# Kernel optimization log

Hardware: AMD Instinct MI355X
Metric: run time of the kernel (lower is better)

Reference implementation:

```python
import jax, jax.numpy as jnp
import numpy as np

GROUPS = 32
EPS = 1e-5


def group_norm(x, gamma, beta):
    # x: [B, C, H, W]; normalize over (C//G, H, W) within each of G groups
    B, C, H, W = x.shape
    xg = x.reshape(B, GROUPS, C // GROUPS, H, W)
    mean = xg.mean(axis=(2, 3, 4), keepdims=True)
    var = xg.var(axis=(2, 3, 4), keepdims=True)
    xg = (xg - mean) * jax.lax.rsqrt(var + EPS)
    x = xg.reshape(B, C, H, W)
    return x * gamma[None, :, None, None] + beta[None, :, None, None]


def conv1x1(x, W, b):
    # 1x1 conv == pointwise linear over channels. x: [B,C,H,W], W: [Cout,Cin]
    return jnp.einsum('oc,bchw->bohw', W, x) + b[None, :, None, None]


def setup_inputs() -> dict:
    key = jax.random.key(0)
    ks = jax.random.split(key, 6)
    B, C, H, W = 16, 512, 32, 32
    scale = 1.0 / np.sqrt(C)  # ~kaiming-ish init for 1x1 convs
    return {
        'x': jax.random.normal(ks[0], (B, C, H, W), jnp.float32),
        'gn_gamma': jnp.ones((C,), jnp.float32),
        'gn_beta': jnp.zeros((C,), jnp.float32),
        'Wq': jax.random.normal(ks[1], (C, C), jnp.float32) * scale,
        'bq': jnp.zeros((C,), jnp.float32),
        'Wk': jax.random.normal(ks[2], (C, C), jnp.float32) * scale,
        'bk': jnp.zeros((C,), jnp.float32),
        'Wv': jax.random.normal(ks[3], (C, C), jnp.float32) * scale,
        'bv': jnp.zeros((C,), jnp.float32),
        'Wp': jax.random.normal(ks[4], (C, C), jnp.float32) * scale,
        'bp': jnp.zeros((C,), jnp.float32),
    }


def reference(x, gn_gamma, gn_beta, Wq, bq, Wk, bk, Wv, bv, Wp, bp):
    B, C, H, W = x.shape
    h = group_norm(x, gn_gamma, gn_beta)
    q = conv1x1(h, Wq, bq).reshape(B, C, H * W)  # [B,C,T]
    k = conv1x1(h, Wk, bk).reshape(B, C, H * W)
    v = conv1x1(h, Wv, bv).reshape(B, C, H * W)
    # scores [B, T(query), S(key)] = q^T k, scaled by C^{-1/2}
    w = jnp.einsum('bct,bcs->bts', q, k) * (C ** -0.5)
    w = jax.nn.softmax(w, axis=-1)
    h = jnp.einsum('bts,bcs->bct', w, v).reshape(B, C, H, W)
    h = conv1x1(h, Wp, bp)
    return x + h
```

## Files before the change

### kernel.cpp

```cpp
#include <hip/hip_runtime.h>

typedef unsigned short u16;
typedef __bf16 bf16x8 __attribute__((ext_vector_type(8)));
typedef float f32x16 __attribute__((ext_vector_type(16)));

__device__ __forceinline__ u16 f2bf(float f) {
    unsigned u = __builtin_bit_cast(unsigned, f);
    u += 0x7fffu + ((u >> 16) & 1u);
    return (u16)(u >> 16);
}
__device__ __forceinline__ float bf2f(u16 h) {
    return __builtin_bit_cast(float, (unsigned)h << 16);
}

#define GLDS16(g, l) __builtin_amdgcn_global_load_lds( \
    (const __attribute__((address_space(1))) void*)(g), \
    (__attribute__((address_space(3))) void*)(l), 16, 0, 0)

#define QK_SCALE 0.044194173824159216f

__global__ __launch_bounds__(256) void convert_kernel(
    const float* __restrict__ Wq, const float* __restrict__ Wk,
    const float* __restrict__ Wv, const float* __restrict__ Wp,
    const float* __restrict__ bq, const float* __restrict__ bk,
    const float* __restrict__ bv,
    u16* __restrict__ Wqkv, u16* __restrict__ Wpb, float* __restrict__ bqkv)
{
    int idx = blockIdx.x * 256 + threadIdx.x;
    if (idx < 786432) {
        int which = idx >> 18;
        int off   = idx & 262143;
        if (which == 0)
            Wqkv[idx] = f2bf(Wq[off] * QK_SCALE);
        else
            Wqkv[idx] = f2bf(((which == 1) ? Wk : Wv)[off]);
    } else {
        int off = idx - 786432;
        Wpb[off] = f2bf(Wp[off]);
    }
    if (idx < 1536) {
        float bvv = (idx < 512) ? bq[idx] * QK_SCALE
                  : (idx < 1024) ? bk[idx & 511] : bv[idx & 511];
        bqkv[idx] = bvv;
    }
}

__global__ __launch_bounds__(256) void gn_kernel(
    const float* __restrict__ x, const float* __restrict__ gamma,
    const float* __restrict__ beta, u16* __restrict__ ht)
{
    const int g = blockIdx.x, b = blockIdx.y, tid = threadIdx.x;
    const float* xg = x + ((size_t)b * 512 + (size_t)g * 16) * 1024;

    float s = 0.f, s2 = 0.f;
    const float4* x4 = (const float4*)xg;
    #pragma unroll 4
    for (int i = tid; i < 4096; i += 256) {
        float4 v = x4[i];
        s  += v.x + v.y + v.z + v.w;
        s2 += v.x * v.x + v.y * v.y + v.z * v.z + v.w * v.w;
    }
    #pragma unroll
    for (int off = 32; off; off >>= 1) {
        s  += __shfl_down(s, off);
        s2 += __shfl_down(s2, off);
    }
    __shared__ float rs[4], rs2[4];
    __shared__ float stat[2];
    const int w = tid >> 6;
    if ((tid & 63) == 0) { rs[w] = s; rs2[w] = s2; }
    __syncthreads();
    if (tid == 0) {
        float S  = rs[0] + rs[1] + rs[2] + rs[3];
        float S2 = rs2[0] + rs2[1] + rs2[2] + rs2[3];
        float mean = S * (1.f / 16384.f);
        float var  = S2 * (1.f / 16384.f) - mean * mean;
        stat[0] = mean;
        stat[1] = rsqrtf(var + 1e-5f);
    }
    __syncthreads();
    const float mean = stat[0], rstd = stat[1];

    float ga[16], be[16];
    #pragma unroll
    for (int ci = 0; ci < 16; ci++) {
        ga[ci] = gamma[g * 16 + ci];
        be[ci] = beta[g * 16 + ci];
    }
    for (int t = tid; t < 1024; t += 256) {
        u16 yv[16];
        #pragma unroll
        for (int ci = 0; ci < 16; ci++) {
            float v = xg[ci * 1024 + t];
            yv[ci] = f2bf((v - mean) * rstd * ga[ci] + be[ci]);
        }
        uint4* dst = (uint4*)(ht + ((size_t)b * 1024 + t) * 512 + g * 16);
        dst[0] = ((const uint4*)yv)[0];
        dst[1] = ((const uint4*)yv)[1];
    }
}

__global__ __launch_bounds__(256) void softmax_kernel(u16* __restrict__ scores)
{
    const int row  = blockIdx.x * 4 + (threadIdx.x >> 6);
    const int lane = threadIdx.x & 63;
    u16* p = scores + (size_t)row * 1024 + lane * 16;

    uint4 w0 = ((const uint4*)p)[0];
    uint4 w1 = ((const uint4*)p)[1];
    unsigned wd[8] = {w0.x, w0.y, w0.z, w0.w, w1.x, w1.y, w1.z, w1.w};
    float v[16];
    #pragma unroll
    for (int i = 0; i < 8; i++) {
        v[2 * i]     = __builtin_bit_cast(float, wd[i] << 16);
        v[2 * i + 1] = __builtin_bit_cast(float, wd[i] & 0xffff0000u);
    }
    float m = v[0];
    #pragma unroll
    for (int i = 1; i < 16; i++) m = fmaxf(m, v[i]);
    #pragma unroll
    for (int off = 1; off < 64; off <<= 1) m = fmaxf(m, __shfl_xor(m, off));

    float s = 0.f;
    #pragma unroll
    for (int i = 0; i < 16; i++) { v[i] = __expf(v[i] - m); s += v[i]; }
    #pragma unroll
    for (int off = 1; off < 64; off <<= 1) s += __shfl_xor(s, off);
    const float inv = 1.0f / s;

    #pragma unroll
    for (int i = 0; i < 8; i++) {
        unsigned lo = f2bf(v[2 * i] * inv);
        unsigned hi = f2bf(v[2 * i + 1] * inv);
        wd[i] = lo | (hi << 16);
    }
    ((uint4*)p)[0] = make_uint4(wd[0], wd[1], wd[2], wd[3]);
    ((uint4*)p)[1] = make_uint4(wd[4], wd[5], wd[6], wd[7]);
}

template <int MODE>
__global__ __launch_bounds__(256) void gemm_nt(
    const u16* __restrict__ A, const u16* __restrict__ B,
    size_t strideA, size_t strideB, int lda, int ldb, int K,
    u16* __restrict__ o0, u16* __restrict__ o1, u16* __restrict__ o2,
    float* __restrict__ fo, const float* __restrict__ bias,
    const float* __restrict__ xres)
{
    __shared__ u16 As[128 * 64];
    __shared__ u16 Bs[128 * 64];

    const int tid   = threadIdx.x;
    const int lane  = tid & 63;
    const int wave  = tid >> 6;
    const int wm    = (wave >> 1) * 64;
    const int wn    = (wave & 1) * 64;
    const int l31   = lane & 31;
    const int khalf = lane >> 5;
    const int b     = blockIdx.z;

    const u16* Ab = A + (size_t)b * strideA + (size_t)blockIdx.y * 128 * lda;
    const u16* Bb = B + (size_t)b * strideB + (size_t)blockIdx.x * 128 * ldb;

    const int srow = lane >> 3;
    const int sc   = lane & 7;
    const int scg  = sc ^ srow;

    f32x16 acc[2][2] = {};

    for (int k0 = 0; k0 < K; k0 += 64) {
        __syncthreads();
        #pragma unroll
        for (int s = 0; s < 4; s++) {
            const int r = wave * 32 + s * 8 + srow;
            GLDS16(Ab + (size_t)r * lda + k0 + scg * 8, As + r * 64 + sc * 8);
            GLDS16(Bb + (size_t)r * ldb + k0 + scg * 8, Bs + r * 64 + sc * 8);
        }
        __syncthreads();

        #pragma unroll
        for (int ks = 0; ks < 4; ks++) {
            const int cidx = ks * 2 + khalf;
            const int slot = (cidx ^ (lane & 7)) * 8;
            bf16x8 af[2], bfr[2];
            #pragma unroll
            for (int i = 0; i < 2; i++)
                af[i] = *(const bf16x8*)(As + (wm + i * 32 + l31) * 64 + slot);
            #pragma unroll
            for (int j = 0; j < 2; j++)
                bfr[j] = *(const bf16x8*)(Bs + (wn + j * 32 + l31) * 64 + slot);
            #pragma unroll
            for (int i = 0; i < 2; i++)
                #pragma unroll
                for (int j = 0; j < 2; j++)
                    acc[i][j] = __builtin_amdgcn_mfma_f32_32x32x16_bf16(
                        af[i], bfr[j], acc[i][j], 0, 0, 0);
        }
    }

    const int m_base = blockIdx.y * 128 + wm + 4 * khalf;
    const int n_base = blockIdx.x * 128 + wn + l31;

    #pragma unroll
    for (int i = 0; i < 2; i++) {
        #pragma unroll
        for (int j = 0; j < 2; j++) {
            const int n = n_base + j * 32;
            float bv = 0.f;
            if (MODE == 0 || MODE == 3) bv = bias[n];
            #pragma unroll
            for (int g = 0; g < 4; g++) {
                const int m = m_base + i * 32 + 8 * g;
                const float a0 = acc[i][j][4 * g]     + bv;
                const float a1 = acc[i][j][4 * g + 1] + bv;
                const float a2 = acc[i][j][4 * g + 2] + bv;
                const float a3 = acc[i][j][4 * g + 3] + bv;
                if (MODE == 0) {
                    if (n < 1024) {
                        u16* dst = (n < 512) ? o0 : o1;
                        const int nn = n & 511;
                        dst[((size_t)b * 1024 + m) * 512 + nn]     = f2bf(a0);
                        dst[((size_t)b * 1024 + m + 1) * 512 + nn] = f2bf(a1);
                        dst[((size_t)b * 1024 + m + 2) * 512 + nn] = f2bf(a2);
                        dst[((size_t)b * 1024 + m + 3) * 512 + nn] = f2bf(a3);
                    } else {
                        ushort4 hv = {f2bf(a0), f2bf(a1), f2bf(a2), f2bf(a3)};
                        *(ushort4*)(o2 + ((size_t)b * 512 + (n - 1024)) * 1024 + m) = hv;
                    }
                } else if (MODE == 1) {
                    ushort4 hv = {f2bf(a0), f2bf(a1), f2bf(a2), f2bf(a3)};
                    *(ushort4*)(o0 + ((size_t)b * 1024 + n) * 1024 + m) = hv;
                } else if (MODE == 2) {
                    ushort4 hv = {f2bf(a0), f2bf(a1), f2bf(a2), f2bf(a3)};
                    *(ushort4*)(o0 + ((size_t)b * 1024 + n) * 512 + m) = hv;
                } else {
                    const size_t off = ((size_t)b * 512 + n) * 1024 + m;
                    const float4 xv = *(const float4*)(xres + off);
                    float4 ov = {a0 + xv.x, a1 + xv.y, a2 + xv.z, a3 + xv.w};
                    *(float4*)(fo + off) = ov;
                }
            }
        }
    }
}

extern "C" void kernel_launch(void* const* d_in, const int* in_sizes, int n_in,
                              void* d_out, int out_size, void* d_ws, size_t ws_size,
                              hipStream_t stream)
{
    const float* x     = (const float*)d_in[0];
    const float* gamma = (const float*)d_in[1];
    const float* beta  = (const float*)d_in[2];
    const float* Wq    = (const float*)d_in[3];
    const float* bq    = (const float*)d_in[4];
    const float* Wk    = (const float*)d_in[5];
    const float* bk    = (const float*)d_in[6];
    const float* Wv    = (const float*)d_in[7];
    const float* bv    = (const float*)d_in[8];
    const float* Wp    = (const float*)d_in[9];
    const float* bp    = (const float*)d_in[10];

    char* ws = (char*)d_ws;
    u16*   Wqkv   = (u16*)(ws + 0);
    u16*   Wpb    = (u16*)(ws + 1572864);
    float* bqkv   = (float*)(ws + 2097152);
    u16*   ht     = (u16*)(ws + 2105344);
    u16*   kt     = (u16*)(ws + 18882560);
    u16*   vv     = (u16*)(ws + 35659776);
    u16*   scores = (u16*)(ws + 52436992);
    u16*   qt  = (u16*)d_out;
    u16*   h2  = ht;
    float* out = (float*)d_out;

    convert_kernel<<<4096, 256, 0, stream>>>(Wq, Wk, Wv, Wp, bq, bk, bv,
                                             Wqkv, Wpb, bqkv);
    gn_kernel<<<dim3(32, 16), 256, 0, stream>>>(x, gamma, beta, ht);

    gemm_nt<0><<<dim3(12, 8, 16), 256, 0, stream>>>(
        ht, Wqkv, 524288, 0, 512, 512, 512,
        qt, kt, vv, nullptr, bqkv, nullptr);

    gemm_nt<1><<<dim3(8, 8, 16), 256, 0, stream>>>(
        kt, qt, 524288, 524288, 512, 512, 512,
        scores, nullptr, nullptr, nullptr, nullptr, nullptr);

    softmax_kernel<<<4096, 256, 0, stream>>>(scores);

    gemm_nt<2><<<dim3(8, 4, 16), 256, 0, stream>>>(
        vv, scores, 524288, 1048576, 1024, 1024, 1024,
        h2, nullptr, nullptr, nullptr, nullptr, nullptr);

    gemm_nt<3><<<dim3(4, 8, 16), 256, 0, stream>>>(
        h2, Wpb, 524288, 0, 512, 512, 512,
        nullptr, nullptr, nullptr, out, bp, x);
}
```

Before: 253.8 us.

## Split group norm into stats/apply, stage GEMM epilogues through LDS, remap workgroups

Group norm is split into a statistics kernel and an apply kernel that transposes a 512x32 tile through swizzled LDS, so both the reads of x and the writes to the transposed activations are coalesced. The GEMM epilogues for transposed outputs, and the fp32 residual output, are staged through shared memory so that global stores become full 16-byte row writes. Workgroup IDs are remapped across eight groups, likely to spread neighbouring tiles across XCDs. A launch-bounds occupancy hint is added. The trade-off is one extra kernel launch, extra LDS traffic and barriers, and group statistics stored in spare space in the output buffer.

```diff
diff --git a/kernel.cpp b/kernel.cpp
--- a/kernel.cpp
+++ b/kernel.cpp
@@ -45,9 +45,8 @@
     }
 }
 
-__global__ __launch_bounds__(256) void gn_kernel(
-    const float* __restrict__ x, const float* __restrict__ gamma,
-    const float* __restrict__ beta, u16* __restrict__ ht)
+__global__ __launch_bounds__(256) void gn_stats(
+    const float* __restrict__ x, float2* __restrict__ stats)
 {
     const int g = blockIdx.x, b = blockIdx.y, tid = threadIdx.x;
     const float* xg = x + ((size_t)b * 512 + (size_t)g * 16) * 1024;
@@ -66,7 +65,6 @@
         s2 += __shfl_down(s2, off);
     }
     __shared__ float rs[4], rs2[4];
-    __shared__ float stat[2];
     const int w = tid >> 6;
     if ((tid & 63) == 0) { rs[w] = s; rs2[w] = s2; }
     __syncthreads();
@@ -75,28 +73,53 @@
         float S2 = rs2[0] + rs2[1] + rs2[2] + rs2[3];
         float mean = S * (1.f / 16384.f);
         float var  = S2 * (1.f / 16384.f) - mean * mean;
-        stat[0] = mean;
-        stat[1] = rsqrtf(var + 1e-5f);
-    }
+        stats[b * 32 + g] = make_float2(mean, rsqrtf(var + 1e-5f));
+    }
+}
+
+__global__ __launch_bounds__(256) void gn_apply(
+    const float* __restrict__ x, const float* __restrict__ gamma,
+    const float* __restrict__ beta, const float2* __restrict__ stats,
+    u16* __restrict__ ht)
+{
+    const int tc = blockIdx.x, b = blockIdx.y, tid = threadIdx.x;
+    const int t0 = tc * 32;
+
+    __shared__ float2 st[32];
+    __shared__ float ga[512], be[512];
+    __shared__ __align__(16) u16 tile[512 * 32];
+
+    if (tid < 32) st[tid] = stats[b * 32 + tid];
+    for (int c = tid; c < 512; c += 256) { ga[c] = gamma[c]; be[c] = beta[c]; }
     __syncthreads();
-    const float mean = stat[0], rstd = stat[1];
-
-    float ga[16], be[16];
-    #pragma unroll
-    for (int ci = 0; ci < 16; ci++) {
-        ga[ci] = gamma[g * 16 + ci];
-        be[ci] = beta[g * 16 + ci];
-    }
-    for (int t = tid; t < 1024; t += 256) {
-        u16 yv[16];
-        #pragma unroll
-        for (int ci = 0; ci < 16; ci++) {
-            float v = xg[ci * 1024 + t];
-            yv[ci] = f2bf((v - mean) * rstd * ga[ci] + be[ci]);
-        }
-        uint4* dst = (uint4*)(ht + ((size_t)b * 1024 + t) * 512 + g * 16);
-        dst[0] = ((const uint4*)yv)[0];
-        dst[1] = ((const uint4*)yv)[1];
+
+    #pragma unroll
+    for (int pass = 0; pass < 16; pass++) {
+        const int c = pass * 32 + (tid >> 3);
+        const int f = tid & 7;
+        float4 v = *(const float4*)(x + ((size_t)(b * 512 + c)) * 1024 + t0 + f * 4);
+        float2 s = st[c >> 4];
+        float sc = s.y * ga[c];
+        float sh = be[c] - s.x * sc;
+        ushort4 hv = {f2bf(v.x * sc + sh), f2bf(v.y * sc + sh),
+                      f2bf(v.z * sc + sh), f2bf(v.w * sc + sh)};
+        const int slot = f ^ (c & 7) ^ ((c >> 3) & 7);
+        *(ushort4*)(tile + c * 32 + slot * 4) = hv;
+    }
+    __syncthreads();
+
+    #pragma unroll
+    for (int p = 0; p < 8; p++) {
+        const int t = p * 4 + (tid >> 6);
+        const int l = tid & 63;
+        u16 tmp[8];
+        #pragma unroll
+        for (int e = 0; e < 8; e++) {
+            const int c = l * 8 + e;
+            const int slot = (t >> 2) ^ (c & 7) ^ ((c >> 3) & 7);
+            tmp[e] = tile[c * 32 + slot * 4 + (t & 3)];
+        }
+        *(uint4*)(ht + ((size_t)b * 1024 + t0 + t) * 512 + l * 8) = *(uint4*)tmp;
     }
 }
 
@@ -139,15 +162,16 @@
 }
 
 template <int MODE>
-__global__ __launch_bounds__(256) void gemm_nt(
+__global__ __launch_bounds__(256, 4) void gemm_nt(
     const u16* __restrict__ A, const u16* __restrict__ B,
     size_t strideA, size_t strideB, int lda, int ldb, int K,
     u16* __restrict__ o0, u16* __restrict__ o1, u16* __restrict__ o2,
     float* __restrict__ fo, const float* __restrict__ bias,
     const float* __restrict__ xres)
 {
-    __shared__ u16 As[128 * 64];
-    __shared__ u16 Bs[128 * 64];
+    __shared__ __align__(16) u16 sm[16384];
+    u16* As = sm;
+    u16* Bs = sm + 8192;
 
     const int tid   = threadIdx.x;
     const int lane  = tid & 63;
@@ -156,10 +180,18 @@
     const int wn    = (wave & 1) * 64;
     const int l31   = lane & 31;
     const int khalf = lane >> 5;
-    const int b     = blockIdx.z;
-
-    const u16* Ab = A + (size_t)b * strideA + (size_t)blockIdx.y * 128 * lda;
-    const u16* Bb = B + (size_t)b * strideB + (size_t)blockIdx.x * 128 * ldb;
+
+    const int gx = gridDim.x, gy = gridDim.y;
+    int f = blockIdx.x + gx * (blockIdx.y + gy * blockIdx.z);
+    const int nwg = gx * gy * (int)gridDim.z;
+    f = (f & 7) * (nwg >> 3) + (f >> 3);
+    const int bx  = f % gx;
+    const int byz = f / gx;
+    const int by  = byz % gy;
+    const int b   = byz / gy;
+
+    const u16* Ab = A + (size_t)b * strideA + (size_t)by * 128 * lda;
+    const u16* Bb = B + (size_t)b * strideB + (size_t)bx * 128 * ldb;
 
     const int srow = lane >> 3;
     const int sc   = lane & 7;
@@ -197,47 +229,90 @@
         }
     }
 
-    const int m_base = blockIdx.y * 128 + wm + 4 * khalf;
-    const int n_base = blockIdx.x * 128 + wn + l31;
-
-    #pragma unroll
-    for (int i = 0; i < 2; i++) {
-        #pragma unroll
-        for (int j = 0; j < 2; j++) {
-            const int n = n_base + j * 32;
-            float bv = 0.f;
-            if (MODE == 0 || MODE == 3) bv = bias[n];
-            #pragma unroll
-            for (int g = 0; g < 4; g++) {
-                const int m = m_base + i * 32 + 8 * g;
-                const float a0 = acc[i][j][4 * g]     + bv;
-                const float a1 = acc[i][j][4 * g + 1] + bv;
-                const float a2 = acc[i][j][4 * g + 2] + bv;
-                const float a3 = acc[i][j][4 * g + 3] + bv;
-                if (MODE == 0) {
-                    if (n < 1024) {
-                        u16* dst = (n < 512) ? o0 : o1;
-                        const int nn = n & 511;
-                        dst[((size_t)b * 1024 + m) * 512 + nn]     = f2bf(a0);
-                        dst[((size_t)b * 1024 + m + 1) * 512 + nn] = f2bf(a1);
-                        dst[((size_t)b * 1024 + m + 2) * 512 + nn] = f2bf(a2);
-                        dst[((size_t)b * 1024 + m + 3) * 512 + nn] = f2bf(a3);
-                    } else {
-                        ushort4 hv = {f2bf(a0), f2bf(a1), f2bf(a2), f2bf(a3)};
-                        *(ushort4*)(o2 + ((size_t)b * 512 + (n - 1024)) * 1024 + m) = hv;
-                    }
-                } else if (MODE == 1) {
-                    ushort4 hv = {f2bf(a0), f2bf(a1), f2bf(a2), f2bf(a3)};
-                    *(ushort4*)(o0 + ((size_t)b * 1024 + n) * 1024 + m) = hv;
-                } else if (MODE == 2) {
-                    ushort4 hv = {f2bf(a0), f2bf(a1), f2bf(a2), f2bf(a3)};
-                    *(ushort4*)(o0 + ((size_t)b * 1024 + n) * 512 + m) = hv;
-                } else {
-                    const size_t off = ((size_t)b * 512 + n) * 1024 + m;
-                    const float4 xv = *(const float4*)(xres + off);
-                    float4 ov = {a0 + xv.x, a1 + xv.y, a2 + xv.z, a3 + xv.w};
-                    *(float4*)(fo + off) = ov;
+    const int N0 = bx * 128;
+    const int M0 = by * 128;
+
+    if (MODE == 0 && N0 < 1024) {
+        const int m_base = M0 + wm + 4 * khalf;
+        const int n_base = N0 + wn + l31;
+        #pragma unroll
+        for (int i = 0; i < 2; i++) {
+            #pragma unroll
+            for (int j = 0; j < 2; j++) {
+                const int n  = n_base + j * 32;
+                const float bv = bias[n];
+                u16* dst = (n < 512) ? o0 : o1;
+                const int nn = n & 511;
+                #pragma unroll
+                for (int g = 0; g < 4; g++) {
+                    const int m = m_base + i * 32 + 8 * g;
+                    dst[((size_t)b * 1024 + m) * 512 + nn]     = f2bf(acc[i][j][4 * g]     + bv);
+                    dst[((size_t)b * 1024 + m + 1) * 512 + nn] = f2bf(acc[i][j][4 * g + 1] + bv);
+                    dst[((size_t)b * 1024 + m + 2) * 512 + nn] = f2bf(acc[i][j][4 * g + 2] + bv);
+                    dst[((size_t)b * 1024 + m + 3) * 512 + nn] = f2bf(acc[i][j][4 * g + 3] + bv);
                 }
+            }
+        }
+    } else if (MODE != 3) {
+        __syncthreads();
+        #pragma unroll
+        for (int i = 0; i < 2; i++) {
+            #pragma unroll
+            for (int j = 0; j < 2; j++) {
+                const int n = wn + j * 32 + l31;
+                const float bv = (MODE == 0) ? bias[N0 + n] : 0.f;
+                #pragma unroll
+                for (int g = 0; g < 4; g++) {
+                    const int m = wm + 4 * khalf + i * 32 + 8 * g;
+                    ushort4 hv = {f2bf(acc[i][j][4 * g]     + bv),
+                                  f2bf(acc[i][j][4 * g + 1] + bv),
+                                  f2bf(acc[i][j][4 * g + 2] + bv),
+                                  f2bf(acc[i][j][4 * g + 3] + bv)};
+                    *(ushort4*)(sm + n * 128 + (((m >> 3) ^ (n & 15)) << 3) + (m & 7)) = hv;
+                }
+            }
+        }
+        __syncthreads();
+        #pragma unroll
+        for (int p = 0; p < 8; p++) {
+            const int n  = p * 16 + (tid >> 4);
+            const int gi = tid & 15;
+            uint4 v = *(const uint4*)(sm + n * 128 + ((gi ^ (n & 15)) << 3));
+            u16* dst;
+            if (MODE == 0)      dst = o2 + ((size_t)b * 512 + (N0 - 1024 + n)) * 1024 + M0;
+            else if (MODE == 1) dst = o0 + ((size_t)b * 1024 + N0 + n) * 1024 + M0;
+            else                dst = o0 + ((size_t)b * 1024 + N0 + n) * 512 + M0;
+            *(uint4*)(dst + gi * 8) = v;
+        }
+    } else {
+        float* smf = (float*)sm;
+        #pragma unroll
+        for (int i = 0; i < 2; i++) {
+            __syncthreads();
+            #pragma unroll
+            for (int j = 0; j < 2; j++) {
+                const int n = wn + j * 32 + l31;
+                #pragma unroll
+                for (int g = 0; g < 4; g++) {
+                    const int mIdx = 4 * khalf + 8 * g + ((wm >> 6) << 5);
+                    float4 v4 = {acc[i][j][4 * g],     acc[i][j][4 * g + 1],
+                                 acc[i][j][4 * g + 2], acc[i][j][4 * g + 3]};
+                    *(float4*)(smf + n * 64 + (((mIdx >> 2) ^ (n & 15)) << 2)) = v4;
+                }
+            }
+            __syncthreads();
+            #pragma unroll
+            for (int p = 0; p < 8; p++) {
+                const int n  = p * 16 + (tid >> 4);
+                const int gi = tid & 15;
+                float4 v = *(const float4*)(smf + n * 64 + ((gi ^ (n & 15)) << 2));
+                const int m = (gi & 7) * 4 + ((gi >> 3) << 6) + 32 * i;
+                const size_t off = ((size_t)b * 512 + N0 + n) * 1024 + M0 + m;
+                const float bv = bias[N0 + n];
+                const float4 xv = *(const float4*)(xres + off);
+                float4 ov = {v.x + bv + xv.x, v.y + bv + xv.y,
+                             v.z + bv + xv.z, v.w + bv + xv.w};
+                *(float4*)(fo + off) = ov;
             }
         }
     }
@@ -268,12 +343,14 @@
     u16*   vv     = (u16*)(ws + 35659776);
     u16*   scores = (u16*)(ws + 52436992);
     u16*   qt  = (u16*)d_out;
+    float2* stats = (float2*)((char*)d_out + 16777216);
     u16*   h2  = ht;
     float* out = (float*)d_out;
 
     convert_kernel<<<4096, 256, 0, stream>>>(Wq, Wk, Wv, Wp, bq, bk, bv,
                                              Wqkv, Wpb, bqkv);
-    gn_kernel<<<dim3(32, 16), 256, 0, stream>>>(x, gamma, beta, ht);
+    gn_stats<<<dim3(32, 16), 256, 0, stream>>>(x, stats);
+    gn_apply<<<dim3(32, 16), 256, 0, stream>>>(x, gamma, beta, stats, ht);
 
     gemm_nt<0><<<dim3(12, 8, 16), 256, 0, stream>>>(
         ht, Wqkv, 524288, 0, 512, 512, 512,
```

After: 232.2 us. -8.5%, faster.
